# Performance work log

Measured on AMD Instinct MI355X. Metric: run time of the kernel, lower is better.

## Reference

```python
import jax, jax.numpy as jnp
import numpy as np

N, E, F_IN, H, C, ED, NODES = 25000, 100000, 16, 4, 280, 6, 6


def setup_inputs() -> dict:
    key = jax.random.key(0)
    ks = jax.random.split(key, 16)
    s = lambda k, sh: jax.random.normal(k, sh, dtype=jnp.float32) * 0.05
    return {
        "x": jax.random.normal(ks[0], (N, F_IN), dtype=jnp.float32),
        "edge_index": jax.random.randint(ks[1], (2, E), 0, N, dtype=jnp.int64),
        "edge_attr": jax.random.normal(ks[2], (E, ED), dtype=jnp.float32),
        # TransformerConv params (PyG): lin_query/key/value (bias), lin_edge (no bias), lin_skip (bias)
        "Wq": s(ks[3], (F_IN, H * C)), "bq": jnp.zeros((H * C,), jnp.float32),
        "Wk": s(ks[4], (F_IN, H * C)), "bk": jnp.zeros((H * C,), jnp.float32),
        "Wv": s(ks[5], (F_IN, H * C)), "bv": jnp.zeros((H * C,), jnp.float32),
        "We": s(ks[6], (ED, H * C)),
        "Wskip": s(ks[7], (F_IN, C)), "bskip": jnp.zeros((C,), jnp.float32),
        # MLP: 280 -> 64 -> 16 -> NODES, softmax
        "W1": s(ks[8], (280, 64)), "b1": jnp.zeros((64,), jnp.float32),
        "W2": s(ks[9], (64, 16)), "b2": jnp.zeros((16,), jnp.float32),
        "W3": s(ks[10], (16, NODES)), "b3": jnp.zeros((NODES,), jnp.float32),
    }


def reference(x, edge_index, edge_attr, Wq, bq, Wk, bk, Wv, bv, We, Wskip, bskip, W1, b1, W2, b2, W3, b3):
    n = x.shape[0]
    src, dst = edge_index[0], edge_index[1]  # message j -> i (PyG convention)
    q = (x @ Wq + bq).reshape(n, H, C)
    k = (x @ Wk + bk).reshape(n, H, C)
    v = (x @ Wv + bv).reshape(n, H, C)
    e = (edge_attr @ We).reshape(-1, H, C)  # [E,H,C]
    kj = k[src] + e                          # gather + edge features
    alpha = jnp.einsum('ehc,ehc->eh', q[dst], kj) / jnp.sqrt(jnp.float32(C))  # [E,H]
    # numerically stable segment softmax over destination nodes
    amax = jax.ops.segment_max(alpha, dst, num_segments=n)
    ex = jnp.exp(alpha - amax[dst])
    denom = jax.ops.segment_sum(ex, dst, num_segments=n)
    attn = ex / (denom[dst] + 1e-16)
    out = jax.ops.segment_sum(attn[..., None] * (v[src] + e), dst, num_segments=n)  # [N,H,C]
    out = out.mean(axis=1)                  # concat=False -> mean over heads
    out = out + x @ Wskip + bskip           # root/skip connection
    h = out.reshape(-1, 280)
    h = jax.nn.relu(h @ W1 + b1)
    h = jax.nn.relu(h @ W2 + b2)
    return jax.nn.softmax(h @ W3 + b3, axis=-1)
```

## Files before the change

### kernel.cpp

```cpp
#include <hip/hip_runtime.h>

#define N_NODES 25000
#define N_EDGES 100000
#define NPAD 25024
#define CH 280
#define HC 1120
#define CAP 32

typedef unsigned int uint;
typedef unsigned short ushort;
typedef __attribute__((ext_vector_type(8))) short short8;
typedef __attribute__((ext_vector_type(4))) float f32x4;

#define FAC_A 0
#define FAC_B 1024
#define FAC_C 1408
#define FAC_D 1472
#define FAC_F 1536
#define FAC_G 1560
#define FAC_TOTAL 1564

#define WC_K 128

#define PREP_FAC_END   25
#define PREP_WC_END    54
#define PREP_W2_END    55
#define PREP_FILL_END  446
#define PREP_TOTAL     544

__device__ __forceinline__ ushort f2bf(float f) {
  union { float f; uint u; } c; c.f = f;
  uint u = c.u + 0x7FFFu + ((c.u >> 16) & 1u);
  return (ushort)(u >> 16);
}

__global__ __launch_bounds__(256) void prep_kernel(
    const float* __restrict__ Wq, const float* __restrict__ Wk,
    const float* __restrict__ We, const float* __restrict__ bq,
    const float* __restrict__ bk, float* __restrict__ fac,
    const float* __restrict__ Wv, const float* __restrict__ bv,
    const float* __restrict__ Wskip, const float* __restrict__ bskip,
    const float* __restrict__ W1, const float* __restrict__ b1,
    ushort* __restrict__ Wct,
    const float* __restrict__ W2, ushort* __restrict__ W2tg,
    const int* __restrict__ ei, const float* __restrict__ ea,
    int* __restrict__ cursor, float* __restrict__ erec,
    const float* __restrict__ x, ushort* __restrict__ Vb) {
  int b = blockIdx.x;
  if (b < PREP_FAC_END) {
    int t4 = b * 256 + threadIdx.x;
    int q = t4 >> 2, li = t4 & 3;
    if (q >= FAC_TOTAL) return;
    const float *pa, *pb;
    if (q < FAC_B) {
      int h = q >> 8, f = (q >> 4) & 15, g = q & 15;
      pa = Wq + f * HC + h * CH; pb = Wk + g * HC + h * CH;
    } else if (q < FAC_C) {
      int u = q - FAC_B; int h = u / 96, v2 = u % 96, f = v2 / 6, j = v2 % 6;
      pa = Wq + f * HC + h * CH; pb = We + j * HC + h * CH;
    } else if (q < FAC_D) {
      int u = q - FAC_C; int h = u >> 4, f = u & 15;
      pa = Wq + f * HC + h * CH; pb = bk + h * CH;
    } else if (q < FAC_F) {
      int u = q - FAC_D; int h = u >> 4, g = u & 15;
      pa = Wk + g * HC + h * CH; pb = bq + h * CH;
    } else if (q < FAC_G) {
      int u = q - FAC_F; int h = u / 6, j = u % 6;
      pa = We + j * HC + h * CH; pb = bq + h * CH;
    } else {
      int h = q - FAC_G;
      pa = bq + h * CH; pb = bk + h * CH;
    }
    float acc = 0.f;
    int c0 = li * 70;
    for (int c = c0; c < c0 + 70; ++c) acc = fmaf(pa[c], pb[c], acc);
    acc += __shfl_xor(acc, 1);
    acc += __shfl_xor(acc, 2);
    if (li == 0) fac[q] = acc;
  } else if (b < PREP_WC_END) {
    int wid = threadIdx.x >> 6;
    int r = __builtin_amdgcn_readfirstlane((b - PREP_FAC_END) * 4 + wid);
    if (r >= 113) return;
    int k = threadIdx.x & 63;
    const float* w = nullptr;
    float scale = 1.f;
    bool zero = false;
    if (r < 96) {
      int h = r / 24, j = r % 24;
      if (j == 23) zero = true;
      else {
        if (j < 16) w = Wv + j * HC + h * CH;
        else if (j < 22) w = We + (j - 16) * HC + h * CH;
        else w = bv + h * CH;
        scale = 0.25f;
      }
    } else if (r < 112) {
      w = Wskip + (r - 96) * CH;
    } else {
      w = bskip;
    }
    if (zero) return;
    float acc = 0.f;
    for (int c = 0; c < CH; ++c) acc = fmaf(w[c], W1[c * 64 + k], acc);
    float v = acc * scale;
    if (r == 112) v += b1[k];
    Wct[k * WC_K + r] = f2bf(v);
  } else if (b < PREP_W2_END) {
    for (int t = threadIdx.x; t < 1024; t += 256) {
      int m2 = t >> 6, k = t & 63;
      W2tg[m2 * 64 + k] = f2bf(W2[(size_t)k * 16 + m2]);
    }
  } else if (b < PREP_FILL_END) {
    int e = (b - PREP_W2_END) * 256 + threadIdx.x;
    if (e >= N_EDGES) return;
    int src = ei[e];
    int dst = ei[N_EDGES + e];
    int pos = atomicAdd(&cursor[dst], 1);
    if (pos >= CAP) return;
    const float2* s2 = (const float2*)(ea + (size_t)e * 6);
    float2 e01 = s2[0], e23 = s2[1], e45 = s2[2];
    int4 w0;
    w0.x = src;
    w0.y = __float_as_int(e01.x); w0.z = __float_as_int(e01.y);
    w0.w = __float_as_int(e23.x);
    float4 w1 = make_float4(e23.y, e45.x, e45.y, 0.f);
    float* dstp = erec + ((size_t)dst * CAP + pos) * 8;
    *(int4*)dstp = w0;
    *(float4*)(dstp + 4) = w1;
  } else {
    int n = (b - PREP_FILL_END) * 256 + threadIdx.x;
    if (n >= N_NODES) return;
    const float4* x4 = (const float4*)(x + (size_t)n * 16);
    float xv[16];
#pragma unroll
    for (int i = 0; i < 4; ++i) {
      float4 q = x4[i];
      xv[4 * i] = q.x; xv[4 * i + 1] = q.y; xv[4 * i + 2] = q.z; xv[4 * i + 3] = q.w;
    }
    uint pk[8];
#pragma unroll
    for (int i = 0; i < 8; ++i)
      pk[i] = (uint)f2bf(xv[2 * i]) | ((uint)f2bf(xv[2 * i + 1]) << 16);
    int4* vp = (int4*)(Vb + (size_t)n * WC_K + 96);
    int4 s0, s1, s2, s3;
    s0.x = (int)pk[0]; s0.y = (int)pk[1]; s0.z = (int)pk[2]; s0.w = (int)pk[3];
    s1.x = (int)pk[4]; s1.y = (int)pk[5]; s1.z = (int)pk[6]; s1.w = (int)pk[7];
    s2.x = (int)0x3F80u; s2.y = 0; s2.z = 0; s2.w = 0;
    s3.x = 0; s3.y = 0; s3.z = 0; s3.w = 0;
    vp[0] = s0; vp[1] = s1; vp[2] = s2; vp[3] = s3;
  }
}

__global__ __launch_bounds__(256) void attn_kernel(
    const float* __restrict__ x, const float* __restrict__ fac,
    const float* __restrict__ erec, const int* __restrict__ cursor,
    ushort* __restrict__ Vb) {
  const float RS = 0.05976143046671968f;
  int h = blockIdx.y;
  int wid = threadIdx.x >> 6, lane = threadIdx.x & 63;
  int sub = lane >> 2, half = lane & 3;
  int n = (blockIdx.x * 4 + wid) * 16 + sub;
  if (n >= N_NODES) return;
  float xv[16];
  {
    const float4* x4 = (const float4*)(x + (size_t)n * 16);
#pragma unroll
    for (int i = 0; i < 4; ++i) {
      float4 q = x4[i];
      xv[4 * i] = q.x; xv[4 * i + 1] = q.y; xv[4 * i + 2] = q.z; xv[4 * i + 3] = q.w;
    }
  }
  const float* A  = fac + FAC_A + h * 256;
  const float* B  = fac + FAC_B + h * 96;
  const float* cf = fac + FAC_C + h * 16;
  const float* df = fac + FAC_D + h * 16;
  const float* ff = fac + FAC_F + h * 6;
  const float  gf = fac[FAC_G + h];
  float va[16];
#pragma unroll
  for (int g = 0; g < 16; ++g) {
    float a = df[g];
#pragma unroll
    for (int f = 0; f < 16; ++f) a = fmaf(xv[f], A[f * 16 + g], a);
    va[g] = a;
  }
  float ve[6];
#pragma unroll
  for (int j = 0; j < 6; ++j) {
    float a = ff[j];
#pragma unroll
    for (int f = 0; f < 16; ++f) a = fmaf(xv[f], B[f * 6 + j], a);
    ve[j] = a;
  }
  float v22 = gf;
#pragma unroll
  for (int f = 0; f < 16; ++f) v22 = fmaf(xv[f], cf[f], v22);

  int dg = cursor[n];
  if (dg > CAP) dg = CAP;
  float m = -1e30f, den = 0.f;
  float Sx[16];
  float Sa[6];
#pragma unroll
  for (int f = 0; f < 16; ++f) Sx[f] = 0.f;
#pragma unroll
  for (int j = 0; j < 6; ++j) Sa[j] = 0.f;
  for (int q2 = half; q2 < dg; q2 += 4) {
    const float* er = erec + ((size_t)n * CAP + q2) * 8;
    int4 ra = *(const int4*)er;
    float4 rb = *(const float4*)(er + 4);
    int s = ra.x;
    const float4* xs4 = (const float4*)(x + (size_t)s * 16);
    float4 a0 = xs4[0], a1 = xs4[1], a2 = xs4[2], a3 = xs4[3];
    float xs[16] = {a0.x, a0.y, a0.z, a0.w, a1.x, a1.y, a1.z, a1.w,
                    a2.x, a2.y, a2.z, a2.w, a3.x, a3.y, a3.z, a3.w};
    float eav[6] = {__int_as_float(ra.y), __int_as_float(ra.z),
                    __int_as_float(ra.w), rb.x, rb.y, rb.z};
    float alpha = v22;
#pragma unroll
    for (int f = 0; f < 16; ++f) alpha = fmaf(va[f], xs[f], alpha);
#pragma unroll
    for (int j = 0; j < 6; ++j) alpha = fmaf(ve[j], eav[j], alpha);
    alpha *= RS;
    float nm = fmaxf(m, alpha);
    float sc = __expf(m - nm);
    float w = __expf(alpha - nm);
    den = den * sc + w;
#pragma unroll
    for (int f = 0; f < 16; ++f) Sx[f] = fmaf(Sx[f], sc, w * xs[f]);
#pragma unroll
    for (int j = 0; j < 6; ++j) Sa[j] = fmaf(Sa[j], sc, w * eav[j]);
    m = nm;
  }
#pragma unroll
  for (int d = 1; d <= 2; d <<= 1) {
    float mo  = __shfl_xor(m, d);
    float dno = __shfl_xor(den, d);
    float mm = fmaxf(m, mo);
    float sa = __expf(m - mm);
    float sb = __expf(mo - mm);
    den = den * sa + dno * sb;
#pragma unroll
    for (int f = 0; f < 16; ++f) {
      float so = __shfl_xor(Sx[f], d);
      Sx[f] = Sx[f] * sa + so * sb;
    }
#pragma unroll
    for (int j = 0; j < 6; ++j) {
      float so = __shfl_xor(Sa[j], d);
      Sa[j] = Sa[j] * sa + so * sb;
    }
    m = mm;
  }
  if (half) return;
  float inv = 1.f / (den + 1e-16f);
  float outv[24];
#pragma unroll
  for (int f = 0; f < 16; ++f) outv[f] = Sx[f] * inv;
#pragma unroll
  for (int j = 0; j < 6; ++j) outv[16 + j] = Sa[j] * inv;
  outv[22] = den * inv;
  outv[23] = 0.f;
  uint pk[12];
#pragma unroll
  for (int i = 0; i < 12; ++i)
    pk[i] = (uint)f2bf(outv[2 * i]) | ((uint)f2bf(outv[2 * i + 1]) << 16);
  int4* vp = (int4*)(Vb + (size_t)n * WC_K + h * 24);
  int4 s0, s1, s2;
  s0.x = (int)pk[0]; s0.y = (int)pk[1]; s0.z = (int)pk[2]; s0.w = (int)pk[3];
  s1.x = (int)pk[4]; s1.y = (int)pk[5]; s1.z = (int)pk[6]; s1.w = (int)pk[7];
  s2.x = (int)pk[8]; s2.y = (int)pk[9]; s2.z = (int)pk[10]; s2.w = (int)pk[11];
  vp[0] = s0; vp[1] = s1; vp[2] = s2;
}

__global__ __launch_bounds__(256) void mlp_kernel(
    const ushort* __restrict__ Vb, const ushort* __restrict__ Wct,
    const ushort* __restrict__ W2tg, const float* __restrict__ b2,
    const float* __restrict__ W3, const float* __restrict__ b3,
    float* __restrict__ out) {
  __shared__ ushort Wcs[64 * 136];
  __shared__ ushort W2ts[16 * 72];
  __shared__ ushort h1b[64 * 72];
  __shared__ float  h2s[64 * 17];
  int tid = threadIdx.x;
  int wid = tid >> 6, lane = tid & 63;
  int col15 = lane & 15, quad = lane >> 4;
  {
    int row = tid >> 2, seg = tid & 3;
    const ushort* src = Wct + row * 128 + seg * 32;
    ushort* dst = Wcs + row * 136 + seg * 32;
#pragma unroll
    for (int i = 0; i < 4; ++i)
      *(int4*)(dst + i * 8) = *(const int4*)(src + i * 8);
  }
  if (tid < 128) {
    int row = tid >> 3, seg = tid & 7;
    *(int4*)(W2ts + row * 72 + seg * 8) = *(const int4*)(W2tg + row * 64 + seg * 8);
  }
  __syncthreads();
  int node = blockIdx.x * 64 + wid * 16 + col15;
  f32x4 acc[4];
#pragma unroll
  for (int T = 0; T < 4; ++T) acc[T] = (f32x4){0.f, 0.f, 0.f, 0.f};
#pragma unroll
  for (int kk = 0; kk < 4; ++kk) {
    int k0 = kk * 32;
    short8 a = *(const short8*)(Vb + (size_t)node * WC_K + k0 + quad * 8);
#pragma unroll
    for (int T = 0; T < 4; ++T) {
      short8 bfr = *(const short8*)(Wcs + (T * 16 + col15) * 136 + k0 + quad * 8);
      acc[T] = __builtin_amdgcn_mfma_f32_16x16x32_bf16(a, bfr, acc[T], 0, 0, 0);
    }
  }
#pragma unroll
  for (int T = 0; T < 4; ++T) {
#pragma unroll
    for (int r = 0; r < 4; ++r) {
      int nloc = wid * 16 + quad * 4 + r;
      int c = T * 16 + col15;
      h1b[nloc * 72 + c] = f2bf(fmaxf(acc[T][r], 0.f));
    }
  }
  __syncthreads();
  float b2v = b2[col15];
  f32x4 acc2 = (f32x4){0.f, 0.f, 0.f, 0.f};
#pragma unroll
  for (int kk = 0; kk < 2; ++kk) {
    int k0 = kk * 32;
    short8 a2 = *(const short8*)(h1b + (wid * 16 + col15) * 72 + k0 + quad * 8);
    short8 bf2 = *(const short8*)(W2ts + col15 * 72 + k0 + quad * 8);
    acc2 = __builtin_amdgcn_mfma_f32_16x16x32_bf16(a2, bf2, acc2, 0, 0, 0);
  }
#pragma unroll
  for (int r = 0; r < 4; ++r) {
    int nloc = wid * 16 + quad * 4 + r;
    h2s[nloc * 17 + col15] = fmaxf(acc2[r] + b2v, 0.f);
  }
  __syncthreads();
  if (tid < 64) {
    int n = blockIdx.x * 64 + tid;
    if (n < N_NODES) {
      float hv[16];
#pragma unroll
      for (int j = 0; j < 16; ++j) hv[j] = h2s[tid * 17 + j];
      float lg[6];
      float mx = -1e30f;
#pragma unroll
      for (int o = 0; o < 6; ++o) {
        float a = b3[o];
#pragma unroll
        for (int j = 0; j < 16; ++j) a = fmaf(hv[j], W3[j * 6 + o], a);
        lg[o] = a; mx = fmaxf(mx, a);
      }
      float s = 0.f;
#pragma unroll
      for (int o = 0; o < 6; ++o) { lg[o] = __expf(lg[o] - mx); s += lg[o]; }
      float inv = 1.f / s;
      float2* o2 = (float2*)(out + (size_t)n * 6);
      o2[0] = make_float2(lg[0] * inv, lg[1] * inv);
      o2[1] = make_float2(lg[2] * inv, lg[3] * inv);
      o2[2] = make_float2(lg[4] * inv, lg[5] * inv);
    }
  }
}

extern "C" void kernel_launch(void* const* d_in, const int* in_sizes, int n_in,
                              void* d_out, int out_size, void* d_ws, size_t ws_size,
                              hipStream_t stream) {
  const float* x     = (const float*)d_in[0];
  const int*   ei    = (const int*)d_in[1];
  const float* ea    = (const float*)d_in[2];
  const float* Wq    = (const float*)d_in[3];
  const float* bq    = (const float*)d_in[4];
  const float* Wk    = (const float*)d_in[5];
  const float* bk    = (const float*)d_in[6];
  const float* Wv    = (const float*)d_in[7];
  const float* bv    = (const float*)d_in[8];
  const float* We    = (const float*)d_in[9];
  const float* Wskip = (const float*)d_in[10];
  const float* bskip = (const float*)d_in[11];
  const float* W1    = (const float*)d_in[12];
  const float* b1    = (const float*)d_in[13];
  const float* W2    = (const float*)d_in[14];
  const float* b2    = (const float*)d_in[15];
  const float* W3    = (const float*)d_in[16];
  const float* b3    = (const float*)d_in[17];
  float* out = (float*)d_out;
  (void)in_sizes; (void)n_in; (void)out_size; (void)ws_size;

  char* ws = (char*)d_ws;
  size_t off = 0;
  auto alloc = [&](size_t bytes) {
    void* p = ws + off;
    off = (off + bytes + 255) & ~(size_t)255;
    return p;
  };
  float*  fac      = (float*)alloc(FAC_TOTAL * 4);
  ushort* Wct      = (ushort*)alloc(64 * WC_K * 2);
  int*    cursor   = (int*)alloc(N_NODES * 4);
  ushort* W2tg     = (ushort*)alloc(16 * 64 * 2);
  ushort* Vb       = (ushort*)alloc((size_t)NPAD * WC_K * 2);
  float*  erec     = (float*)alloc((size_t)N_NODES * CAP * 8 * 4);

  hipMemsetAsync(Wct, 0, 64 * WC_K * 2 + N_NODES * 4, stream);
  prep_kernel<<<PREP_TOTAL, 256, 0, stream>>>(
      Wq, Wk, We, bq, bk, fac, Wv, bv, Wskip, bskip, W1, b1, Wct, W2, W2tg,
      ei, ea, cursor, erec, x, Vb);
  attn_kernel<<<dim3(391, 4), 256, 0, stream>>>(x, fac, erec, cursor, Vb);
  mlp_kernel<<<391, 256, 0, stream>>>(Vb, Wct, W2tg, b2, W3, b3, out);
}
```

Measured before the change: 125.9 us.

## Fuse attention aggregation into MLP kernel via shared-memory staging

Merges the attention and MLP kernels into one. Each block handles 64 nodes, and each wave computes one head with one thread per node, walking that node's edges serially instead of splitting them across 4 lanes with shuffle reductions. The per-node bf16 aggregate row is written to LDS instead of a global Vb buffer. This removes a kernel launch and the global write and reread of Vb, and the prep kernel no longer fills the x part of Vb. In exchange, per-thread work rises fourfold with serial edge loops, and only 391 blocks launch, giving lower parallelism for the gather phase.

```diff
diff --git a/kernel.cpp b/kernel.cpp
--- a/kernel.cpp
+++ b/kernel.cpp
@@ -2,7 +2,6 @@
 
 #define N_NODES 25000
 #define N_EDGES 100000
-#define NPAD 25024
 #define CH 280
 #define HC 1120
 #define CAP 32
@@ -22,11 +21,10 @@
 
 #define WC_K 128
 
-#define PREP_FAC_END   25
-#define PREP_WC_END    54
-#define PREP_W2_END    55
-#define PREP_FILL_END  446
-#define PREP_TOTAL     544
+#define P_FAC_END  25
+#define P_WC_END   57
+#define P_W2_END   58
+#define P_TOTAL    449
 
 __device__ __forceinline__ ushort f2bf(float f) {
   union { float f; uint u; } c; c.f = f;
@@ -44,11 +42,11 @@
     ushort* __restrict__ Wct,
     const float* __restrict__ W2, ushort* __restrict__ W2tg,
     const int* __restrict__ ei, const float* __restrict__ ea,
-    int* __restrict__ cursor, float* __restrict__ erec,
-    const float* __restrict__ x, ushort* __restrict__ Vb) {
+    int* __restrict__ cursor, float* __restrict__ erec) {
   int b = blockIdx.x;
-  if (b < PREP_FAC_END) {
-    int t4 = b * 256 + threadIdx.x;
+  int tid = threadIdx.x;
+  if (b < P_FAC_END) {
+    int t4 = b * 256 + tid;
     int q = t4 >> 2, li = t4 & 3;
     if (q >= FAC_TOTAL) return;
     const float *pa, *pb;
@@ -77,41 +75,46 @@
     acc += __shfl_xor(acc, 1);
     acc += __shfl_xor(acc, 2);
     if (li == 0) fac[q] = acc;
-  } else if (b < PREP_WC_END) {
-    int wid = threadIdx.x >> 6;
-    int r = __builtin_amdgcn_readfirstlane((b - PREP_FAC_END) * 4 + wid);
-    if (r >= 113) return;
-    int k = threadIdx.x & 63;
-    const float* w = nullptr;
-    float scale = 1.f;
-    bool zero = false;
-    if (r < 96) {
-      int h = r / 24, j = r % 24;
-      if (j == 23) zero = true;
-      else {
-        if (j < 16) w = Wv + j * HC + h * CH;
-        else if (j < 22) w = We + (j - 16) * HC + h * CH;
-        else w = bv + h * CH;
-        scale = 0.25f;
+  } else if (b < P_WC_END) {
+    int wid = tid >> 6;
+    int r = __builtin_amdgcn_readfirstlane((b - P_FAC_END) * 4 + wid);
+    int k = tid & 63;
+    float v = 0.f;
+    bool wz = true;
+    if (r < 113) {
+      const float* w = nullptr;
+      float scale = 1.f;
+      bool zero = false;
+      if (r < 96) {
+        int h = r / 24, j = r % 24;
+        if (j == 23) zero = true;
+        else {
+          if (j < 16) w = Wv + j * HC + h * CH;
+          else if (j < 22) w = We + (j - 16) * HC + h * CH;
+          else w = bv + h * CH;
+          scale = 0.25f;
+        }
+      } else if (r < 112) {
+        w = Wskip + (r - 96) * CH;
+      } else {
+        w = bskip;
       }
-    } else if (r < 112) {
-      w = Wskip + (r - 96) * CH;
-    } else {
-      w = bskip;
-    }
-    if (zero) return;
-    float acc = 0.f;
-    for (int c = 0; c < CH; ++c) acc = fmaf(w[c], W1[c * 64 + k], acc);
-    float v = acc * scale;
-    if (r == 112) v += b1[k];
-    Wct[k * WC_K + r] = f2bf(v);
-  } else if (b < PREP_W2_END) {
-    for (int t = threadIdx.x; t < 1024; t += 256) {
+      if (!zero) {
+        float acc = 0.f;
+        for (int c = 0; c < CH; ++c) acc = fmaf(w[c], W1[c * 64 + k], acc);
+        v = acc * scale;
+        if (r == 112) v += b1[k];
+        wz = false;
+      }
+    }
+    Wct[k * WC_K + r] = wz ? (ushort)0 : f2bf(v);
+  } else if (b < P_W2_END) {
+    for (int t = tid; t < 1024; t += 256) {
       int m2 = t >> 6, k = t & 63;
       W2tg[m2 * 64 + k] = f2bf(W2[(size_t)k * 16 + m2]);
     }
-  } else if (b < PREP_FILL_END) {
-    int e = (b - PREP_W2_END) * 256 + threadIdx.x;
+  } else {
+    int e = (b - P_W2_END) * 256 + tid;
     if (e >= N_EDGES) return;
     int src = ei[e];
     int dst = ei[N_EDGES + e];
@@ -127,51 +130,52 @@
     float* dstp = erec + ((size_t)dst * CAP + pos) * 8;
     *(int4*)dstp = w0;
     *(float4*)(dstp + 4) = w1;
-  } else {
-    int n = (b - PREP_FILL_END) * 256 + threadIdx.x;
-    if (n >= N_NODES) return;
+  }
+}
+
+__global__ __launch_bounds__(256, 2) void fused_kernel(
+    const float* __restrict__ x, const float* __restrict__ fac,
+    const float* __restrict__ erec, const int* __restrict__ cursor,
+    const ushort* __restrict__ Wct, const ushort* __restrict__ W2tg,
+    const float* __restrict__ b2, const float* __restrict__ W3,
+    const float* __restrict__ b3, float* __restrict__ out) {
+  __shared__ ushort Vls[64 * 136];
+  __shared__ ushort Wcs[64 * 136];
+  __shared__ ushort W2ts[16 * 72];
+  __shared__ ushort h1b[64 * 72];
+  __shared__ float  h2s[64 * 17];
+  const float RS = 0.05976143046671968f;
+  int tid = threadIdx.x;
+  int wid = tid >> 6, lane = tid & 63;
+  int h = __builtin_amdgcn_readfirstlane(wid);
+
+  {
+    int row = tid >> 2, seg = tid & 3;
+    const ushort* src = Wct + row * 128 + seg * 32;
+    ushort* dst = Wcs + row * 136 + seg * 32;
+#pragma unroll
+    for (int i = 0; i < 4; ++i)
+      *(int4*)(dst + i * 8) = *(const int4*)(src + i * 8);
+  }
+  if (tid < 128) {
+    int row = tid >> 3, seg = tid & 7;
+    *(int4*)(W2ts + row * 72 + seg * 8) = *(const int4*)(W2tg + row * 64 + seg * 8);
+  }
+
+  int n0 = blockIdx.x * 64 + lane;
+  bool valid = n0 < N_NODES;
+  int n = valid ? n0 : (N_NODES - 1);
+  float xv[16];
+  {
     const float4* x4 = (const float4*)(x + (size_t)n * 16);
-    float xv[16];
 #pragma unroll
     for (int i = 0; i < 4; ++i) {
       float4 q = x4[i];
       xv[4 * i] = q.x; xv[4 * i + 1] = q.y; xv[4 * i + 2] = q.z; xv[4 * i + 3] = q.w;
     }
-    uint pk[8];
-#pragma unroll
-    for (int i = 0; i < 8; ++i)
-      pk[i] = (uint)f2bf(xv[2 * i]) | ((uint)f2bf(xv[2 * i + 1]) << 16);
-    int4* vp = (int4*)(Vb + (size_t)n * WC_K + 96);
-    int4 s0, s1, s2, s3;
-    s0.x = (int)pk[0]; s0.y = (int)pk[1]; s0.z = (int)pk[2]; s0.w = (int)pk[3];
-    s1.x = (int)pk[4]; s1.y = (int)pk[5]; s1.z = (int)pk[6]; s1.w = (int)pk[7];
-    s2.x = (int)0x3F80u; s2.y = 0; s2.z = 0; s2.w = 0;
-    s3.x = 0; s3.y = 0; s3.z = 0; s3.w = 0;
-    vp[0] = s0; vp[1] = s1; vp[2] = s2; vp[3] = s3;
-  }
-}
-
-__global__ __launch_bounds__(256) void attn_kernel(
-    const float* __restrict__ x, const float* __restrict__ fac,
-    const float* __restrict__ erec, const int* __restrict__ cursor,
-    ushort* __restrict__ Vb) {
-  const float RS = 0.05976143046671968f;
-  int h = blockIdx.y;
-  int wid = threadIdx.x >> 6, lane = threadIdx.x & 63;
-  int sub = lane >> 2, half = lane & 3;
-  int n = (blockIdx.x * 4 + wid) * 16 + sub;
-  if (n >= N_NODES) return;
-  float xv[16];
-  {
-    const float4* x4 = (const float4*)(x + (size_t)n * 16);
-#pragma unroll
-    for (int i = 0; i < 4; ++i) {
-      float4 q = x4[i];
-      xv[4 * i] = q.x; xv[4 * i + 1] = q.y; xv[4 * i + 2] = q.z; xv[4 * i + 3] = q.w;
-    }
-  }
-  const float* A  = fac + FAC_A + h * 256;
-  const float* B  = fac + FAC_B + h * 96;
+  }
+  const float* Af = fac + FAC_A + h * 256;
+  const float* Bf = fac + FAC_B + h * 96;
   const float* cf = fac + FAC_C + h * 16;
   const float* df = fac + FAC_D + h * 16;
   const float* ff = fac + FAC_F + h * 6;
@@ -181,7 +185,7 @@
   for (int g = 0; g < 16; ++g) {
     float a = df[g];
 #pragma unroll
-    for (int f = 0; f < 16; ++f) a = fmaf(xv[f], A[f * 16 + g], a);
+    for (int f = 0; f < 16; ++f) a = fmaf(xv[f], Af[f * 16 + g], a);
     va[g] = a;
   }
   float ve[6];
@@ -189,14 +193,14 @@
   for (int j = 0; j < 6; ++j) {
     float a = ff[j];
 #pragma unroll
-    for (int f = 0; f < 16; ++f) a = fmaf(xv[f], B[f * 6 + j], a);
+    for (int f = 0; f < 16; ++f) a = fmaf(xv[f], Bf[f * 6 + j], a);
     ve[j] = a;
   }
   float v22 = gf;
 #pragma unroll
   for (int f = 0; f < 16; ++f) v22 = fmaf(xv[f], cf[f], v22);
 
-  int dg = cursor[n];
+  int dg = valid ? cursor[n0] : 0;
   if (dg > CAP) dg = CAP;
   float m = -1e30f, den = 0.f;
   float Sx[16];
@@ -205,8 +209,8 @@
   for (int f = 0; f < 16; ++f) Sx[f] = 0.f;
 #pragma unroll
   for (int j = 0; j < 6; ++j) Sa[j] = 0.f;
-  for (int q2 = half; q2 < dg; q2 += 4) {
-    const float* er = erec + ((size_t)n * CAP + q2) * 8;
+  for (int q2 = 0; q2 < dg; ++q2) {
+    const float* er = erec + ((size_t)n0 * CAP + q2) * 8;
     int4 ra = *(const int4*)er;
     float4 rb = *(const float4*)(er + 4);
     int s = ra.x;
@@ -232,80 +236,49 @@
     for (int j = 0; j < 6; ++j) Sa[j] = fmaf(Sa[j], sc, w * eav[j]);
     m = nm;
   }
-#pragma unroll
-  for (int d = 1; d <= 2; d <<= 1) {
-    float mo  = __shfl_xor(m, d);
-    float dno = __shfl_xor(den, d);
-    float mm = fmaxf(m, mo);
-    float sa = __expf(m - mm);
-    float sb = __expf(mo - mm);
-    den = den * sa + dno * sb;
-#pragma unroll
-    for (int f = 0; f < 16; ++f) {
-      float so = __shfl_xor(Sx[f], d);
-      Sx[f] = Sx[f] * sa + so * sb;
-    }
-#pragma unroll
-    for (int j = 0; j < 6; ++j) {
-      float so = __shfl_xor(Sa[j], d);
-      Sa[j] = Sa[j] * sa + so * sb;
-    }
-    m = mm;
-  }
-  if (half) return;
-  float inv = 1.f / (den + 1e-16f);
-  float outv[24];
-#pragma unroll
-  for (int f = 0; f < 16; ++f) outv[f] = Sx[f] * inv;
-#pragma unroll
-  for (int j = 0; j < 6; ++j) outv[16 + j] = Sa[j] * inv;
-  outv[22] = den * inv;
-  outv[23] = 0.f;
-  uint pk[12];
-#pragma unroll
-  for (int i = 0; i < 12; ++i)
-    pk[i] = (uint)f2bf(outv[2 * i]) | ((uint)f2bf(outv[2 * i + 1]) << 16);
-  int4* vp = (int4*)(Vb + (size_t)n * WC_K + h * 24);
-  int4 s0, s1, s2;
-  s0.x = (int)pk[0]; s0.y = (int)pk[1]; s0.z = (int)pk[2]; s0.w = (int)pk[3];
-  s1.x = (int)pk[4]; s1.y = (int)pk[5]; s1.z = (int)pk[6]; s1.w = (int)pk[7];
-  s2.x = (int)pk[8]; s2.y = (int)pk[9]; s2.z = (int)pk[10]; s2.w = (int)pk[11];
-  vp[0] = s0; vp[1] = s1; vp[2] = s2;
-}
-
-__global__ __launch_bounds__(256) void mlp_kernel(
-    const ushort* __restrict__ Vb, const ushort* __restrict__ Wct,
-    const ushort* __restrict__ W2tg, const float* __restrict__ b2,
-    const float* __restrict__ W3, const float* __restrict__ b3,
-    float* __restrict__ out) {
-  __shared__ ushort Wcs[64 * 136];
-  __shared__ ushort W2ts[16 * 72];
-  __shared__ ushort h1b[64 * 72];
-  __shared__ float  h2s[64 * 17];
-  int tid = threadIdx.x;
-  int wid = tid >> 6, lane = tid & 63;
+  {
+    float inv = 1.f / (den + 1e-16f);
+    float outv[24];
+#pragma unroll
+    for (int f = 0; f < 16; ++f) outv[f] = Sx[f] * inv;
+#pragma unroll
+    for (int j = 0; j < 6; ++j) outv[16 + j] = Sa[j] * inv;
+    outv[22] = den * inv;
+    outv[23] = 0.f;
+    uint pk[12];
+#pragma unroll
+    for (int i = 0; i < 12; ++i)
+      pk[i] = (uint)f2bf(outv[2 * i]) | ((uint)f2bf(outv[2 * i + 1]) << 16);
+    int4* vp = (int4*)(Vls + lane * 136 + h * 24);
+    int4 s0, s1, s2;
+    s0.x = (int)pk[0]; s0.y = (int)pk[1]; s0.z = (int)pk[2]; s0.w = (int)pk[3];
+    s1.x = (int)pk[4]; s1.y = (int)pk[5]; s1.z = (int)pk[6]; s1.w = (int)pk[7];
+    s2.x = (int)pk[8]; s2.y = (int)pk[9]; s2.z = (int)pk[10]; s2.w = (int)pk[11];
+    vp[0] = s0; vp[1] = s1; vp[2] = s2;
+  }
+  if (wid == 0) {
+    uint pk[8];
+#pragma unroll
+    for (int i = 0; i < 8; ++i)
+      pk[i] = (uint)f2bf(xv[2 * i]) | ((uint)f2bf(xv[2 * i + 1]) << 16);
+    int4* vp = (int4*)(Vls + lane * 136 + 96);
+    int4 s0, s1, s2, s3;
+    s0.x = (int)pk[0]; s0.y = (int)pk[1]; s0.z = (int)pk[2]; s0.w = (int)pk[3];
+    s1.x = (int)pk[4]; s1.y = (int)pk[5]; s1.z = (int)pk[6]; s1.w = (int)pk[7];
+    s2.x = (int)0x3F80u; s2.y = 0; s2.z = 0; s2.w = 0;
+    s3.x = 0; s3.y = 0; s3.z = 0; s3.w = 0;
+    vp[0] = s0; vp[1] = s1; vp[2] = s2; vp[3] = s3;
+  }
+  __syncthreads();
+
   int col15 = lane & 15, quad = lane >> 4;
-  {
-    int row = tid >> 2, seg = tid & 3;
-    const ushort* src = Wct + row * 128 + seg * 32;
-    ushort* dst = Wcs + row * 136 + seg * 32;
-#pragma unroll
-    for (int i = 0; i < 4; ++i)
-      *(int4*)(dst + i * 8) = *(const int4*)(src + i * 8);
-  }
-  if (tid < 128) {
-    int row = tid >> 3, seg = tid & 7;
-    *(int4*)(W2ts + row * 72 + seg * 8) = *(const int4*)(W2tg + row * 64 + seg * 8);
-  }
-  __syncthreads();
-  int node = blockIdx.x * 64 + wid * 16 + col15;
   f32x4 acc[4];
 #pragma unroll
   for (int T = 0; T < 4; ++T) acc[T] = (f32x4){0.f, 0.f, 0.f, 0.f};
 #pragma unroll
   for (int kk = 0; kk < 4; ++kk) {
     int k0 = kk * 32;
-    short8 a = *(const short8*)(Vb + (size_t)node * WC_K + k0 + quad * 8);
+    short8 a = *(const short8*)(Vls + (wid * 16 + col15) * 136 + k0 + quad * 8);
 #pragma unroll
     for (int T = 0; T < 4; ++T) {
       short8 bfr = *(const short8*)(Wcs + (T * 16 + col15) * 136 + k0 + quad * 8);
@@ -338,8 +311,8 @@
   }
   __syncthreads();
   if (tid < 64) {
-    int n = blockIdx.x * 64 + tid;
-    if (n < N_NODES) {
+    int n2 = blockIdx.x * 64 + tid;
+    if (n2 < N_NODES) {
       float hv[16];
 #pragma unroll
       for (int j = 0; j < 16; ++j) hv[j] = h2s[tid * 17 + j];
@@ -356,7 +329,7 @@
 #pragma unroll
       for (int o = 0; o < 6; ++o) { lg[o] = __expf(lg[o] - mx); s += lg[o]; }
       float inv = 1.f / s;
-      float2* o2 = (float2*)(out + (size_t)n * 6);
+      float2* o2 = (float2*)(out + (size_t)n2 * 6);
       o2[0] = make_float2(lg[0] * inv, lg[1] * inv);
       o2[1] = make_float2(lg[2] * inv, lg[3] * inv);
       o2[2] = make_float2(lg[4] * inv, lg[5] * inv);
@@ -395,17 +368,16 @@
     off = (off + bytes + 255) & ~(size_t)255;
     return p;
   };
-  float*  fac      = (float*)alloc(FAC_TOTAL * 4);
-  ushort* Wct      = (ushort*)alloc(64 * WC_K * 2);
-  int*    cursor   = (int*)alloc(N_NODES * 4);
-  ushort* W2tg     = (ushort*)alloc(16 * 64 * 2);
-  ushort* Vb       = (ushort*)alloc((size_t)NPAD * WC_K * 2);
-  float*  erec     = (float*)alloc((size_t)N_NODES * CAP * 8 * 4);
-
-  hipMemsetAsync(Wct, 0, 64 * WC_K * 2 + N_NODES * 4, stream);
-  prep_kernel<<<PREP_TOTAL, 256, 0, stream>>>(
+  float*  fac    = (float*)alloc(FAC_TOTAL * 4);
+  ushort* Wct    = (ushort*)alloc(64 * WC_K * 2);
+  int*    cursor = (int*)alloc(N_NODES * 4);
+  ushort* W2tg   = (ushort*)alloc(16 * 64 * 2);
+  float*  erec   = (float*)alloc((size_t)N_NODES * CAP * 8 * 4);
+
+  hipMemsetAsync(cursor, 0, N_NODES * 4, stream);
+  prep_kernel<<<P_TOTAL, 256, 0, stream>>>(
       Wq, Wk, We, bq, bk, fac, Wv, bv, Wskip, bskip, W1, b1, Wct, W2, W2tg,
-      ei, ea, cursor, erec, x, Vb);
-  attn_kernel<<<dim3(391, 4), 256, 0, stream>>>(x, fac, erec, cursor, Vb);
-  mlp_kernel<<<391, 256, 0, stream>>>(Vb, Wct, W2tg, b2, W3, b3, out);
+      ei, ea, cursor, erec);
+  fused_kernel<<<391, 256, 0, stream>>>(x, fac, erec, cursor, Wct, W2tg,
+                                        b2, W3, b3, out);
 }
```

Result: faster. 118.1 us (-6.2%).
